# Performance work log

Measured on AMD Instinct MI355X. Metric: run time of the kernel, lower is better.

Reference implementation:

```python
import jax, jax.numpy as jnp
import numpy as np

B, T, D, UNITS = 32, 2048, 1024, 1024


def setup_inputs() -> dict:
    key = jax.random.key(0)
    ks = jax.random.split(key, 9)
    values = jax.random.normal(ks[0], (B, T, D), dtype=jnp.float32)
    query = jax.random.normal(ks[1], (B, D), dtype=jnp.float32)
    # mask: 1.0 where position is masked out, 0.0 otherwise
    mask = jax.random.randint(ks[2], (B, T), 0, 2).astype(jnp.float32)
    # Dense params (keras Dense: y = x @ W + b)
    W1 = jax.random.normal(ks[3], (D, UNITS), dtype=jnp.float32) / np.sqrt(D)
    b1 = jnp.zeros((UNITS,), dtype=jnp.float32)
    W2 = jax.random.normal(ks[4], (D, UNITS), dtype=jnp.float32) / np.sqrt(D)
    b2 = jnp.zeros((UNITS,), dtype=jnp.float32)
    V = jax.random.normal(ks[5], (UNITS, 1), dtype=jnp.float32) / np.sqrt(UNITS)
    bV = jnp.zeros((1,), dtype=jnp.float32)
    return {"values": values, "query": query, "mask": mask,
            "W1": W1, "b1": b1, "W2": W2, "b2": b2, "V": V, "bV": bV}


def reference(values, query, mask, W1, b1, W2, b2, V, bV):
    # values: [B,T,D], query: [B,D], mask: [B,T] (1.0 = masked)
    proj_v = jnp.einsum('btd,du->btu', values, W1) + b1          # [B,T,U]
    proj_q = (query @ W2 + b2)[:, None, :]                        # [B,1,U]
    score = jnp.tanh(proj_v + proj_q) @ V + bV                    # [B,T,1]
    score = score + mask[:, :, None] * (-1e9)                     # mask out
    attention_weights = jax.nn.softmax(score, axis=1)             # [B,T,1]
    context_vector = jnp.sum(attention_weights * values, axis=1)  # [B,D]
    return (context_vector, attention_weights)
```

## Files before the change

### kernel.cpp

```cpp
#include <hip/hip_runtime.h>
#include <hip/hip_bf16.h>


typedef __bf16 bf16x8 __attribute__((ext_vector_type(8)));
typedef __bf16 bf16x4 __attribute__((ext_vector_type(4)));
typedef float  f32x4  __attribute__((ext_vector_type(4)));

#define B_  32
#define T_  2048
#define D_  1024
#define U_  1024
#define BT_ (B_*T_)

#define WS_W1T    ((size_t)0)
#define WS_PROJQ  ((size_t)(2u*1024*1024))
#define WS_SCORE  ((size_t)(2u*1024*1024 + 128u*1024))
#define WS_VALB   ((size_t)(4u*1024*1024))
#define WS_NEEDED (WS_VALB + (size_t)BT_ * D_ * 2)

__device__ __forceinline__ float tanh_fast(float x) {
    const float e = __expf(2.0f * x);
    return 1.0f - __fdividef(2.0f, e + 1.0f);
}

__device__ __forceinline__ void glls16(const void* g, void* l) {
    __builtin_amdgcn_global_load_lds(
        (const __attribute__((address_space(1))) void*)g,
        (__attribute__((address_space(3))) void*)l, 16, 0, 0);
}

__global__ void init_kernel(const float* __restrict__ b1, const float* __restrict__ b2,
                            float* __restrict__ projq, float* __restrict__ score) {
    int i = blockIdx.x * 256 + threadIdx.x;
    if (i < B_ * U_) {
        projq[i] = b1[i & (U_ - 1)] + b2[i & (U_ - 1)];
    } else {
        score[i - B_ * U_] = 0.0f;
    }
}

__global__ void convert_kernel(const float* __restrict__ v, __bf16* __restrict__ o) {
    const size_t i = ((size_t)blockIdx.x * 256 + threadIdx.x) * 8;
    const float4 a = *(const float4*)(v + i);
    const float4 b = *(const float4*)(v + i + 4);
    bf16x8 h;
    h[0] = (__bf16)a.x; h[1] = (__bf16)a.y; h[2] = (__bf16)a.z; h[3] = (__bf16)a.w;
    h[4] = (__bf16)b.x; h[5] = (__bf16)b.y; h[6] = (__bf16)b.z; h[7] = (__bf16)b.w;
    *(bf16x8*)(o + i) = h;
}

__global__ void w1_transpose_kernel(const float* __restrict__ W1, __bf16* __restrict__ W1T) {
    __shared__ float tile[64][65];
    const int bx = blockIdx.x & 15;
    const int by = blockIdx.x >> 4;
    const int tid = threadIdx.x;
    const int j  = tid & 63;
    const int i0 = tid >> 6;
#pragma unroll
    for (int p = 0; p < 16; ++p) {
        const int i = i0 + p * 4;
        tile[i][j] = W1[(size_t)(by * 64 + i) * U_ + bx * 64 + j];
    }
    __syncthreads();
#pragma unroll
    for (int p = 0; p < 16; ++p) {
        const int i = i0 + p * 4;
        W1T[(size_t)(bx * 64 + i) * D_ + by * 64 + j] = (__bf16)tile[j][i];
    }
}

__global__ void projq_kernel(const float* __restrict__ query, const float* __restrict__ W2,
                             float* __restrict__ projq) {
    __shared__ float q[128];
    const int b  = blockIdx.x >> 3;
    const int dc = blockIdx.x & 7;
    const int tid = threadIdx.x;
    if (tid < 128) q[tid] = query[(size_t)b * D_ + dc * 128 + tid];
    __syncthreads();
    const int u0 = tid * 4;
    float a0 = 0.f, a1 = 0.f, a2 = 0.f, a3 = 0.f;
    for (int d = 0; d < 128; ++d) {
        const float4 w = *(const float4*)(W2 + (size_t)(dc * 128 + d) * U_ + u0);
        const float qd = q[d];
        a0 = fmaf(qd, w.x, a0); a1 = fmaf(qd, w.y, a1);
        a2 = fmaf(qd, w.z, a2); a3 = fmaf(qd, w.w, a3);
    }
    float* p = projq + (size_t)b * U_ + u0;
    atomicAdd(p + 0, a0); atomicAdd(p + 1, a1);
    atomicAdd(p + 2, a2); atomicAdd(p + 3, a3);
}

__global__ __launch_bounds__(256, 4)
void score_kernel_bf16(const __bf16* __restrict__ valb, const __bf16* __restrict__ W1T,
                       const float* __restrict__ projq, const float* __restrict__ V,
                       float* __restrict__ score) {
    __shared__ __attribute__((aligned(16))) __bf16 Al[128 * 32];
    __shared__ __attribute__((aligned(16))) __bf16 Bl[128 * 32];

    const int tid = threadIdx.x;
    const int xcd  = blockIdx.x & 7;
    const int slot = blockIdx.x >> 3;
    const int rowblk = xcd * 64 + (slot >> 3);
    const int utile  = slot & 7;
    const int wave = tid >> 6, lane = tid & 63;
    const int quad = lane >> 4, l15 = lane & 15;
    const int wr = (wave >> 1) * 64;
    const int wc = (wave & 1) * 64;

    const __bf16* Ab = valb + ((size_t)rowblk * 128 + (tid >> 2)) * D_ + (tid & 3) * 8;
    const __bf16* Bb = W1T + ((size_t)utile * 128 + (tid >> 2)) * D_ + (tid & 3) * 8;
    __bf16* Ald = Al + wave * 512;
    __bf16* Bld = Bl + wave * 512;

    f32x4 acc[4][4];
#pragma unroll
    for (int i = 0; i < 4; ++i)
#pragma unroll
        for (int j = 0; j < 4; ++j) {
            f32x4 z = {0.f, 0.f, 0.f, 0.f};
            acc[i][j] = z;
        }

    for (int kk = 0; kk < D_; kk += 32) {
        glls16(Ab + kk,            Ald);
        glls16(Ab + 64 * D_ + kk,  Ald + 2048);
        glls16(Bb + kk,            Bld);
        glls16(Bb + 64 * D_ + kk,  Bld + 2048);
        __syncthreads();

        bf16x8 af[4];
#pragma unroll
        for (int mt = 0; mt < 4; ++mt)
            af[mt] = *(const bf16x8*)(Al + (wr + mt * 16 + l15) * 32 + quad * 8);
#pragma unroll
        for (int nt = 0; nt < 4; ++nt) {
            const bf16x8 bfr = *(const bf16x8*)(Bl + (wc + nt * 16 + l15) * 32 + quad * 8);
#pragma unroll
            for (int mt = 0; mt < 4; ++mt)
                acc[mt][nt] = __builtin_amdgcn_mfma_f32_16x16x32_bf16(af[mt], bfr, acc[mt][nt], 0, 0, 0);
        }
        __syncthreads();
    }

    const int b = rowblk >> 4;
    const float* pq = projq + (size_t)b * U_ + utile * 128 + wc;
    const float* Vp = V + utile * 128 + wc;
    const size_t rowbase = (size_t)rowblk * 128 + wr;
#pragma unroll
    for (int mt = 0; mt < 4; ++mt) {
        float s0 = 0.f, s1 = 0.f, s2 = 0.f, s3 = 0.f;
#pragma unroll
        for (int nt = 0; nt < 4; ++nt) {
            const int u = nt * 16 + l15;
            const float pqu = pq[u];
            const float vu  = Vp[u];
            s0 += tanh_fast(acc[mt][nt][0] + pqu) * vu;
            s1 += tanh_fast(acc[mt][nt][1] + pqu) * vu;
            s2 += tanh_fast(acc[mt][nt][2] + pqu) * vu;
            s3 += tanh_fast(acc[mt][nt][3] + pqu) * vu;
        }
        float s[4] = {s0, s1, s2, s3};
#pragma unroll
        for (int r = 0; r < 4; ++r) {
            float v = s[r];
            v += __shfl_xor(v, 1);
            v += __shfl_xor(v, 2);
            v += __shfl_xor(v, 4);
            v += __shfl_xor(v, 8);
            if (l15 == 0)
                atomicAdd(&score[rowbase + mt * 16 + quad * 4 + r], v);
        }
    }
}

__global__ __launch_bounds__(512, 2)
void score_kernel_f32(const float* __restrict__ values, const __bf16* __restrict__ W1T,
                      const float* __restrict__ projq, const float* __restrict__ V,
                      float* __restrict__ score) {
    __shared__ __attribute__((aligned(16))) __bf16 Al[64][40];
    __shared__ __attribute__((aligned(16))) __bf16 Bl[512][40];
    const int tid    = threadIdx.x;
    const int rowblk = blockIdx.x >> 1;
    const int nhalf  = blockIdx.x & 1;
    const int wave = tid >> 6, lane = tid & 63;
    const int quad = lane >> 4, l15 = lane & 15;
    const float*  Abase = values + (size_t)rowblk * 64 * D_;
    const __bf16* Bbase = W1T + (size_t)nhalf * 512 * D_;
    const int ar = tid >> 3, ac = (tid & 7) * 4;
    const int br = tid >> 2, bc = (tid & 3) * 8;
    f32x4 acc[4][4];
#pragma unroll
    for (int i = 0; i < 4; ++i)
#pragma unroll
        for (int j = 0; j < 4; ++j) { f32x4 z = {0.f,0.f,0.f,0.f}; acc[i][j] = z; }
    for (int kk = 0; kk < D_; kk += 32) {
        {
            const float4 v = *(const float4*)(Abase + (size_t)ar * D_ + kk + ac);
            bf16x4 h;
            h[0] = (__bf16)v.x; h[1] = (__bf16)v.y; h[2] = (__bf16)v.z; h[3] = (__bf16)v.w;
            *(bf16x4*)(&Al[ar][ac]) = h;
        }
#pragma unroll
        for (int p = 0; p < 4; ++p) {
            const int rr = p * 128 + br;
            const bf16x8 w = *(const bf16x8*)(Bbase + (size_t)rr * D_ + kk + bc);
            *(bf16x8*)(&Bl[rr][bc]) = w;
        }
        __syncthreads();
        bf16x8 af[4];
#pragma unroll
        for (int mt = 0; mt < 4; ++mt)
            af[mt] = *(const bf16x8*)(&Al[mt * 16 + l15][quad * 8]);
#pragma unroll
        for (int nt = 0; nt < 4; ++nt) {
            const bf16x8 bfr = *(const bf16x8*)(&Bl[wave * 64 + nt * 16 + l15][quad * 8]);
#pragma unroll
            for (int mt = 0; mt < 4; ++mt)
                acc[mt][nt] = __builtin_amdgcn_mfma_f32_16x16x32_bf16(af[mt], bfr, acc[mt][nt], 0, 0, 0);
        }
        __syncthreads();
    }
    const int b = rowblk >> 5;
    const size_t rowbase = (size_t)rowblk * 64;
    const float* pq = projq + (size_t)b * U_;
    const int ub = nhalf * 512 + wave * 64;
#pragma unroll
    for (int mt = 0; mt < 4; ++mt) {
        float s0 = 0.f, s1 = 0.f, s2 = 0.f, s3 = 0.f;
#pragma unroll
        for (int nt = 0; nt < 4; ++nt) {
            const int u = ub + nt * 16 + l15;
            const float pqu = pq[u];
            const float vu  = V[u];
            s0 += tanh_fast(acc[mt][nt][0] + pqu) * vu;
            s1 += tanh_fast(acc[mt][nt][1] + pqu) * vu;
            s2 += tanh_fast(acc[mt][nt][2] + pqu) * vu;
            s3 += tanh_fast(acc[mt][nt][3] + pqu) * vu;
        }
        float s[4] = {s0, s1, s2, s3};
#pragma unroll
        for (int r = 0; r < 4; ++r) {
            float v = s[r];
            v += __shfl_xor(v, 1);
            v += __shfl_xor(v, 2);
            v += __shfl_xor(v, 4);
            v += __shfl_xor(v, 8);
            if (l15 == 0)
                atomicAdd(&score[rowbase + mt * 16 + quad * 4 + r], v);
        }
    }
}

__global__ void softmax_kernel(const float* __restrict__ score, const float* __restrict__ mask,
                               const float* __restrict__ bV, float* __restrict__ out) {
    const int b = blockIdx.x;
    const int tid = threadIdx.x;
    const float bv = bV[0];
    float s[8];
    float lmax = -3.0e38f;
#pragma unroll
    for (int i = 0; i < 8; ++i) {
        const int t = tid + i * 256;
        const float v = score[(size_t)b * T_ + t] + bv + mask[(size_t)b * T_ + t] * (-1.0e9f);
        s[i] = v;
        lmax = fmaxf(lmax, v);
    }
#pragma unroll
    for (int m = 1; m < 64; m <<= 1) lmax = fmaxf(lmax, __shfl_xor(lmax, m));
    __shared__ float redm[4], reds[4];
    if ((tid & 63) == 0) redm[tid >> 6] = lmax;
    __syncthreads();
    const float M = fmaxf(fmaxf(redm[0], redm[1]), fmaxf(redm[2], redm[3]));
    float lsum = 0.f;
#pragma unroll
    for (int i = 0; i < 8; ++i) { s[i] = __expf(s[i] - M); lsum += s[i]; }
#pragma unroll
    for (int m = 1; m < 64; m <<= 1) lsum += __shfl_xor(lsum, m);
    if ((tid & 63) == 0) reds[tid >> 6] = lsum;
    __syncthreads();
    const float inv = 1.0f / (reds[0] + reds[1] + reds[2] + reds[3]);
#pragma unroll
    for (int i = 0; i < 8; ++i)
        out[(size_t)B_ * D_ + (size_t)b * T_ + tid + i * 256] = s[i] * inv;
}

__global__ void context_kernel(const float* __restrict__ values, const float* __restrict__ attn,
                               float* __restrict__ out) {
    const int b  = blockIdx.x >> 4;
    const int dc = blockIdx.x & 15;
    const int tid = threadIdx.x;
    __shared__ float a[T_];
#pragma unroll
    for (int i = 0; i < 8; ++i) a[tid + i * 256] = attn[(size_t)b * T_ + tid + i * 256];
    __syncthreads();
    const int dl = (tid & 15) * 4;
    const int tg = tid >> 4;
    const float* vb = values + (size_t)b * T_ * D_ + dc * 64 + dl;
    f32x4 acc = {0.f, 0.f, 0.f, 0.f};
#pragma unroll 4
    for (int t = tg; t < T_; t += 16) {
        const float4 v = *(const float4*)(vb + (size_t)t * D_);
        const float w = a[t];
        acc[0] = fmaf(w, v.x, acc[0]);
        acc[1] = fmaf(w, v.y, acc[1]);
        acc[2] = fmaf(w, v.z, acc[2]);
        acc[3] = fmaf(w, v.w, acc[3]);
    }
    __shared__ __attribute__((aligned(16))) float red[16][64];
    *(f32x4*)(&red[tg][dl]) = acc;
    __syncthreads();
    if (tid < 64) {
        float s = 0.f;
#pragma unroll
        for (int g = 0; g < 16; ++g) s += red[g][tid];
        out[(size_t)b * D_ + dc * 64 + tid] = s;
    }
}

extern "C" void kernel_launch(void* const* d_in, const int* in_sizes, int n_in,
                              void* d_out, int out_size, void* d_ws, size_t ws_size,
                              hipStream_t stream) {
    const float* values = (const float*)d_in[0];
    const float* query  = (const float*)d_in[1];
    const float* mask   = (const float*)d_in[2];
    const float* W1     = (const float*)d_in[3];
    const float* b1     = (const float*)d_in[4];
    const float* W2     = (const float*)d_in[5];
    const float* b2     = (const float*)d_in[6];
    const float* V      = (const float*)d_in[7];
    const float* bV     = (const float*)d_in[8];
    float* out = (float*)d_out;

    char* ws = (char*)d_ws;
    __bf16* W1T   = (__bf16*)(ws + WS_W1T);
    float*  projq = (float*)(ws + WS_PROJQ);
    float*  score = (float*)(ws + WS_SCORE);
    __bf16* valb  = (__bf16*)(ws + WS_VALB);

    init_kernel<<<dim3(384), dim3(256), 0, stream>>>(b1, b2, projq, score);
    w1_transpose_kernel<<<dim3(256), dim3(256), 0, stream>>>(W1, W1T);
    projq_kernel<<<dim3(256), dim3(256), 0, stream>>>(query, W2, projq);
    if (ws_size >= WS_NEEDED) {
        convert_kernel<<<dim3(32768), dim3(256), 0, stream>>>(values, valb);
        score_kernel_bf16<<<dim3(4096), dim3(256), 0, stream>>>(valb, W1T, projq, V, score);
    } else {
        score_kernel_f32<<<dim3(2048), dim3(512), 0, stream>>>(values, W1T, projq, V, score);
    }
    softmax_kernel<<<dim3(32), dim3(256), 0, stream>>>(score, mask, bV, out);
    context_kernel<<<dim3(512), dim3(256), 0, stream>>>(values, out + B_ * D_, out);
}
```

Measured before the change: 634.8 us.

## Switch score GEMM to 32x32x16 MFMA and fold bias init into projq

The bf16 score GEMM now uses 32x32x16 MFMA tiles (2x2 per wave) instead of 16x16x32 (4x4), which cuts LDS fragment loads per k-step and changes the epilogue to a 32-lane reduction with a different row mapping. The init kernel is replaced by a memset of the score buffer, and projq is computed without atomics by having each block cover the full D for 512 units, with the biases added directly. Launch bounds drop to 3 blocks per SM because of the larger accumulator fragments, which may reduce occupancy.

```diff
diff --git a/kernel.cpp b/kernel.cpp
--- a/kernel.cpp
+++ b/kernel.cpp
@@ -5,6 +5,7 @@
 typedef __bf16 bf16x8 __attribute__((ext_vector_type(8)));
 typedef __bf16 bf16x4 __attribute__((ext_vector_type(4)));
 typedef float  f32x4  __attribute__((ext_vector_type(4)));
+typedef float  f32x16 __attribute__((ext_vector_type(16)));
 
 #define B_  32
 #define T_  2048
@@ -27,16 +28,6 @@
     __builtin_amdgcn_global_load_lds(
         (const __attribute__((address_space(1))) void*)g,
         (__attribute__((address_space(3))) void*)l, 16, 0, 0);
-}
-
-__global__ void init_kernel(const float* __restrict__ b1, const float* __restrict__ b2,
-                            float* __restrict__ projq, float* __restrict__ score) {
-    int i = blockIdx.x * 256 + threadIdx.x;
-    if (i < B_ * U_) {
-        projq[i] = b1[i & (U_ - 1)] + b2[i & (U_ - 1)];
-    } else {
-        score[i - B_ * U_] = 0.0f;
-    }
 }
 
 __global__ void convert_kernel(const float* __restrict__ v, __bf16* __restrict__ o) {
@@ -70,27 +61,28 @@
 }
 
 __global__ void projq_kernel(const float* __restrict__ query, const float* __restrict__ W2,
+                             const float* __restrict__ b1, const float* __restrict__ b2,
                              float* __restrict__ projq) {
-    __shared__ float q[128];
-    const int b  = blockIdx.x >> 3;
-    const int dc = blockIdx.x & 7;
-    const int tid = threadIdx.x;
-    if (tid < 128) q[tid] = query[(size_t)b * D_ + dc * 128 + tid];
-    __syncthreads();
-    const int u0 = tid * 4;
-    float a0 = 0.f, a1 = 0.f, a2 = 0.f, a3 = 0.f;
-    for (int d = 0; d < 128; ++d) {
-        const float4 w = *(const float4*)(W2 + (size_t)(dc * 128 + d) * U_ + u0);
+    __shared__ float q[D_];
+    const int b  = blockIdx.x >> 1;
+    const int uc = blockIdx.x & 1;
+    const int tid = threadIdx.x;
+    *(float4*)(q + tid * 4) = *(const float4*)(query + (size_t)b * D_ + tid * 4);
+    __syncthreads();
+    const int u0 = uc * 512 + tid * 2;
+    float a0 = b1[u0] + b2[u0];
+    float a1 = b1[u0 + 1] + b2[u0 + 1];
+#pragma unroll 8
+    for (int d = 0; d < D_; ++d) {
+        const float2 w = *(const float2*)(W2 + (size_t)d * U_ + u0);
         const float qd = q[d];
-        a0 = fmaf(qd, w.x, a0); a1 = fmaf(qd, w.y, a1);
-        a2 = fmaf(qd, w.z, a2); a3 = fmaf(qd, w.w, a3);
-    }
-    float* p = projq + (size_t)b * U_ + u0;
-    atomicAdd(p + 0, a0); atomicAdd(p + 1, a1);
-    atomicAdd(p + 2, a2); atomicAdd(p + 3, a3);
-}
-
-__global__ __launch_bounds__(256, 4)
+        a0 = fmaf(qd, w.x, a0);
+        a1 = fmaf(qd, w.y, a1);
+    }
+    *(float2*)(projq + (size_t)b * U_ + u0) = make_float2(a0, a1);
+}
+
+__global__ __launch_bounds__(256, 3)
 void score_kernel_bf16(const __bf16* __restrict__ valb, const __bf16* __restrict__ W1T,
                        const float* __restrict__ projq, const float* __restrict__ V,
                        float* __restrict__ score) {
@@ -103,7 +95,7 @@
     const int rowblk = xcd * 64 + (slot >> 3);
     const int utile  = slot & 7;
     const int wave = tid >> 6, lane = tid & 63;
-    const int quad = lane >> 4, l15 = lane & 15;
+    const int l31 = lane & 31, half = lane >> 5;
     const int wr = (wave >> 1) * 64;
     const int wc = (wave & 1) * 64;
 
@@ -112,14 +104,14 @@
     __bf16* Ald = Al + wave * 512;
     __bf16* Bld = Bl + wave * 512;
 
-    f32x4 acc[4][4];
-#pragma unroll
-    for (int i = 0; i < 4; ++i)
-#pragma unroll
-        for (int j = 0; j < 4; ++j) {
-            f32x4 z = {0.f, 0.f, 0.f, 0.f};
-            acc[i][j] = z;
-        }
+    f32x16 acc[2][2];
+#pragma unroll
+    for (int i = 0; i < 2; ++i)
+#pragma unroll
+        for (int j = 0; j < 2; ++j)
+#pragma unroll
+            for (int r = 0; r < 16; ++r)
+                acc[i][j][r] = 0.f;
 
     for (int kk = 0; kk < D_; kk += 32) {
         glls16(Ab + kk,            Ald);
@@ -128,17 +120,25 @@
         glls16(Bb + 64 * D_ + kk,  Bld + 2048);
         __syncthreads();
 
-        bf16x8 af[4];
-#pragma unroll
-        for (int mt = 0; mt < 4; ++mt)
-            af[mt] = *(const bf16x8*)(Al + (wr + mt * 16 + l15) * 32 + quad * 8);
-#pragma unroll
-        for (int nt = 0; nt < 4; ++nt) {
-            const bf16x8 bfr = *(const bf16x8*)(Bl + (wc + nt * 16 + l15) * 32 + quad * 8);
-#pragma unroll
-            for (int mt = 0; mt < 4; ++mt)
-                acc[mt][nt] = __builtin_amdgcn_mfma_f32_16x16x32_bf16(af[mt], bfr, acc[mt][nt], 0, 0, 0);
-        }
+        bf16x8 af[2][2], bfr[2][2];
+#pragma unroll
+        for (int mb = 0; mb < 2; ++mb)
+#pragma unroll
+            for (int ks = 0; ks < 2; ++ks)
+                af[mb][ks] = *(const bf16x8*)(Al + (wr + mb * 32 + l31) * 32 + ks * 16 + half * 8);
+#pragma unroll
+        for (int nb = 0; nb < 2; ++nb)
+#pragma unroll
+            for (int ks = 0; ks < 2; ++ks)
+                bfr[nb][ks] = *(const bf16x8*)(Bl + (wc + nb * 32 + l31) * 32 + ks * 16 + half * 8);
+#pragma unroll
+        for (int mb = 0; mb < 2; ++mb)
+#pragma unroll
+            for (int nb = 0; nb < 2; ++nb)
+#pragma unroll
+                for (int ks = 0; ks < 2; ++ks)
+                    acc[mb][nb] = __builtin_amdgcn_mfma_f32_32x32x16_bf16(
+                        af[mb][ks], bfr[nb][ks], acc[mb][nb], 0, 0, 0);
         __syncthreads();
     }
 
@@ -147,28 +147,31 @@
     const float* Vp = V + utile * 128 + wc;
     const size_t rowbase = (size_t)rowblk * 128 + wr;
 #pragma unroll
-    for (int mt = 0; mt < 4; ++mt) {
-        float s0 = 0.f, s1 = 0.f, s2 = 0.f, s3 = 0.f;
-#pragma unroll
-        for (int nt = 0; nt < 4; ++nt) {
-            const int u = nt * 16 + l15;
+    for (int mb = 0; mb < 2; ++mb) {
+        float s[16];
+#pragma unroll
+        for (int r = 0; r < 16; ++r) s[r] = 0.f;
+#pragma unroll
+        for (int nb = 0; nb < 2; ++nb) {
+            const int u = nb * 32 + l31;
             const float pqu = pq[u];
             const float vu  = Vp[u];
-            s0 += tanh_fast(acc[mt][nt][0] + pqu) * vu;
-            s1 += tanh_fast(acc[mt][nt][1] + pqu) * vu;
-            s2 += tanh_fast(acc[mt][nt][2] + pqu) * vu;
-            s3 += tanh_fast(acc[mt][nt][3] + pqu) * vu;
-        }
-        float s[4] = {s0, s1, s2, s3};
-#pragma unroll
-        for (int r = 0; r < 4; ++r) {
+#pragma unroll
+            for (int r = 0; r < 16; ++r)
+                s[r] += tanh_fast(acc[mb][nb][r] + pqu) * vu;
+        }
+#pragma unroll
+        for (int r = 0; r < 16; ++r) {
             float v = s[r];
             v += __shfl_xor(v, 1);
             v += __shfl_xor(v, 2);
             v += __shfl_xor(v, 4);
             v += __shfl_xor(v, 8);
-            if (l15 == 0)
-                atomicAdd(&score[rowbase + mt * 16 + quad * 4 + r], v);
+            v += __shfl_xor(v, 16);
+            if (l31 == 0) {
+                const int row = mb * 32 + (r & 3) + 8 * (r >> 2) + 4 * half;
+                atomicAdd(&score[rowbase + row], v);
+            }
         }
     }
 }
@@ -337,9 +340,9 @@
     float*  score = (float*)(ws + WS_SCORE);
     __bf16* valb  = (__bf16*)(ws + WS_VALB);
 
-    init_kernel<<<dim3(384), dim3(256), 0, stream>>>(b1, b2, projq, score);
+    hipMemsetAsync(score, 0, (size_t)BT_ * sizeof(float), stream);
     w1_transpose_kernel<<<dim3(256), dim3(256), 0, stream>>>(W1, W1T);
-    projq_kernel<<<dim3(256), dim3(256), 0, stream>>>(query, W2, projq);
+    projq_kernel<<<dim3(64), dim3(256), 0, stream>>>(query, W2, b1, b2, projq);
     if (ws_size >= WS_NEEDED) {
         convert_kernel<<<dim3(32768), dim3(256), 0, stream>>>(values, valb);
         score_kernel_bf16<<<dim3(4096), dim3(256), 0, stream>>>(valb, W1T, projq, V, score);
```

Measured after the change: 757.7 us. 19.4% more time.

## Split context reduction over time chunks and remove atomics from query projection

Applied to the files above, without the earlier changes.

The context sum now runs as two stages. Each block computes a partial over a 64-step time chunk using full rows, the partials go into reused workspace, and a second kernel reduces them. The query projection gives each thread one output column over the full depth, folds in both biases, and drops the atomics and the init kernel, which becomes a memset of the score buffer. The launch-bounds occupancy hint on the score GEMM drops from 4 to 3 blocks per SM. The cost is an extra 4MB of partials traffic and one extra launch, and register pressure in the GEMM changes.

```diff
diff --git a/kernel.cpp b/kernel.cpp
--- a/kernel.cpp
+++ b/kernel.cpp
@@ -15,6 +15,7 @@
 #define WS_W1T    ((size_t)0)
 #define WS_PROJQ  ((size_t)(2u*1024*1024))
 #define WS_SCORE  ((size_t)(2u*1024*1024 + 128u*1024))
+#define WS_CTXP   ((size_t)0)
 #define WS_VALB   ((size_t)(4u*1024*1024))
 #define WS_NEEDED (WS_VALB + (size_t)BT_ * D_ * 2)
 
@@ -27,16 +28,6 @@
     __builtin_amdgcn_global_load_lds(
         (const __attribute__((address_space(1))) void*)g,
         (__attribute__((address_space(3))) void*)l, 16, 0, 0);
-}
-
-__global__ void init_kernel(const float* __restrict__ b1, const float* __restrict__ b2,
-                            float* __restrict__ projq, float* __restrict__ score) {
-    int i = blockIdx.x * 256 + threadIdx.x;
-    if (i < B_ * U_) {
-        projq[i] = b1[i & (U_ - 1)] + b2[i & (U_ - 1)];
-    } else {
-        score[i - B_ * U_] = 0.0f;
-    }
 }
 
 __global__ void convert_kernel(const float* __restrict__ v, __bf16* __restrict__ o) {
@@ -70,27 +61,23 @@
 }
 
 __global__ void projq_kernel(const float* __restrict__ query, const float* __restrict__ W2,
+                             const float* __restrict__ b1, const float* __restrict__ b2,
                              float* __restrict__ projq) {
-    __shared__ float q[128];
-    const int b  = blockIdx.x >> 3;
-    const int dc = blockIdx.x & 7;
-    const int tid = threadIdx.x;
-    if (tid < 128) q[tid] = query[(size_t)b * D_ + dc * 128 + tid];
-    __syncthreads();
-    const int u0 = tid * 4;
-    float a0 = 0.f, a1 = 0.f, a2 = 0.f, a3 = 0.f;
-    for (int d = 0; d < 128; ++d) {
-        const float4 w = *(const float4*)(W2 + (size_t)(dc * 128 + d) * U_ + u0);
-        const float qd = q[d];
-        a0 = fmaf(qd, w.x, a0); a1 = fmaf(qd, w.y, a1);
-        a2 = fmaf(qd, w.z, a2); a3 = fmaf(qd, w.w, a3);
-    }
-    float* p = projq + (size_t)b * U_ + u0;
-    atomicAdd(p + 0, a0); atomicAdd(p + 1, a1);
-    atomicAdd(p + 2, a2); atomicAdd(p + 3, a3);
-}
-
-__global__ __launch_bounds__(256, 4)
+    __shared__ float q[D_];
+    const int b  = blockIdx.x >> 2;
+    const int uc = blockIdx.x & 3;
+    const int tid = threadIdx.x;
+    *(float4*)(q + tid * 4) = *(const float4*)(query + (size_t)b * D_ + tid * 4);
+    __syncthreads();
+    const int u0 = uc * 256 + tid;
+    float a0 = b1[u0] + b2[u0];
+#pragma unroll 8
+    for (int d = 0; d < D_; ++d)
+        a0 = fmaf(q[d], W2[(size_t)d * U_ + u0], a0);
+    projq[(size_t)b * U_ + u0] = a0;
+}
+
+__global__ __launch_bounds__(256, 3)
 void score_kernel_bf16(const __bf16* __restrict__ valb, const __bf16* __restrict__ W1T,
                        const float* __restrict__ projq, const float* __restrict__ V,
                        float* __restrict__ score) {
@@ -284,37 +271,36 @@
         out[(size_t)B_ * D_ + (size_t)b * T_ + tid + i * 256] = s[i] * inv;
 }
 
-__global__ void context_kernel(const float* __restrict__ values, const float* __restrict__ attn,
-                               float* __restrict__ out) {
-    const int b  = blockIdx.x >> 4;
-    const int dc = blockIdx.x & 15;
-    const int tid = threadIdx.x;
-    __shared__ float a[T_];
-#pragma unroll
-    for (int i = 0; i < 8; ++i) a[tid + i * 256] = attn[(size_t)b * T_ + tid + i * 256];
-    __syncthreads();
-    const int dl = (tid & 15) * 4;
-    const int tg = tid >> 4;
-    const float* vb = values + (size_t)b * T_ * D_ + dc * 64 + dl;
+__global__ __launch_bounds__(256)
+void context1_kernel(const float* __restrict__ values, const float* __restrict__ attn,
+                     float* __restrict__ ctxp) {
+    const int b  = blockIdx.x >> 5;
+    const int tc = blockIdx.x & 31;
+    const int tid = threadIdx.x;
+    __shared__ float sa[64];
+    if (tid < 64) sa[tid] = attn[(size_t)b * T_ + tc * 64 + tid];
+    __syncthreads();
+    const int d0 = tid * 4;
+    const float* vb = values + ((size_t)b * T_ + tc * 64) * D_ + d0;
     f32x4 acc = {0.f, 0.f, 0.f, 0.f};
-#pragma unroll 4
-    for (int t = tg; t < T_; t += 16) {
+#pragma unroll 8
+    for (int t = 0; t < 64; ++t) {
         const float4 v = *(const float4*)(vb + (size_t)t * D_);
-        const float w = a[t];
+        const float w = sa[t];
         acc[0] = fmaf(w, v.x, acc[0]);
         acc[1] = fmaf(w, v.y, acc[1]);
         acc[2] = fmaf(w, v.z, acc[2]);
         acc[3] = fmaf(w, v.w, acc[3]);
     }
-    __shared__ __attribute__((aligned(16))) float red[16][64];
-    *(f32x4*)(&red[tg][dl]) = acc;
-    __syncthreads();
-    if (tid < 64) {
-        float s = 0.f;
-#pragma unroll
-        for (int g = 0; g < 16; ++g) s += red[g][tid];
-        out[(size_t)b * D_ + dc * 64 + tid] = s;
-    }
+    *(f32x4*)(ctxp + ((size_t)tc * B_ + b) * D_ + d0) = acc;
+}
+
+__global__ void context2_kernel(const float* __restrict__ ctxp, float* __restrict__ out) {
+    const int i = blockIdx.x * 256 + threadIdx.x;
+    float s = 0.f;
+#pragma unroll
+    for (int tc = 0; tc < 32; ++tc) s += ctxp[(size_t)tc * (B_ * D_) + i];
+    out[i] = s;
 }
 
 extern "C" void kernel_launch(void* const* d_in, const int* in_sizes, int n_in,
@@ -335,11 +321,12 @@
     __bf16* W1T   = (__bf16*)(ws + WS_W1T);
     float*  projq = (float*)(ws + WS_PROJQ);
     float*  score = (float*)(ws + WS_SCORE);
+    float*  ctxp  = (float*)(ws + WS_CTXP);
     __bf16* valb  = (__bf16*)(ws + WS_VALB);
 
-    init_kernel<<<dim3(384), dim3(256), 0, stream>>>(b1, b2, projq, score);
+    hipMemsetAsync(score, 0, (size_t)BT_ * sizeof(float), stream);
     w1_transpose_kernel<<<dim3(256), dim3(256), 0, stream>>>(W1, W1T);
-    projq_kernel<<<dim3(256), dim3(256), 0, stream>>>(query, W2, projq);
+    projq_kernel<<<dim3(128), dim3(256), 0, stream>>>(query, W2, b1, b2, projq);
     if (ws_size >= WS_NEEDED) {
         convert_kernel<<<dim3(32768), dim3(256), 0, stream>>>(values, valb);
         score_kernel_bf16<<<dim3(4096), dim3(256), 0, stream>>>(valb, W1T, projq, V, score);
@@ -347,5 +334,6 @@
         score_kernel_f32<<<dim3(2048), dim3(512), 0, stream>>>(values, W1T, projq, V, score);
     }
     softmax_kernel<<<dim3(32), dim3(256), 0, stream>>>(score, mask, bV, out);
-    context_kernel<<<dim3(512), dim3(256), 0, stream>>>(values, out + B_ * D_, out);
-}
+    context1_kernel<<<dim3(1024), dim3(256), 0, stream>>>(values, out + B_ * D_, ctxp);
+    context2_kernel<<<dim3(128), dim3(256), 0, stream>>>(ctxp, out);
+}
```

Measured after the change: 691.6 us. 1.09x slower.
